# Kernel optimization log

Hardware: AMD Instinct MI355X
Metric: run time of the kernel (lower is better)

The kernel has to match this reference:

```python
import jax, jax.numpy as jnp
import numpy as np
import math


def setup_inputs() -> dict:
    key = jax.random.key(0)
    k1, = jax.random.split(key, 1)
    B, C, N = 64, 128, 4096
    x = jax.random.normal(k1, (B, C, N), dtype=jnp.float32)
    return {
        "x": x,
        "log_peak_width": jnp.asarray(math.log(3.0), dtype=jnp.float32),
        "log_valley_width": jnp.asarray(math.log(3.0), dtype=jnp.float32),
    }


def reference(x, log_peak_width, log_valley_width):
    # x: (B, C, N)
    B, C, N = x.shape
    diff = jnp.diff(x, axis=-1)                      # (B, C, N-1)
    sign_change = jnp.sign(jnp.diff(diff, axis=-1))  # (B, C, N-2)

    # Torch code gathers ALL nonzero positions across (B, C) flattened and sums
    # one gaussian bump per occurrence. Equivalent, jit-friendly form: count
    # occurrences per center position, then weight one gaussian row per center.
    peak_counts = (sign_change < 0).sum(axis=(0, 1)).astype(x.dtype)    # (N-2,)
    valley_counts = (sign_change > 0).sum(axis=(0, 1)).astype(x.dtype)  # (N-2,)

    pos = jnp.arange(N, dtype=x.dtype)               # (N,)
    centers = jnp.arange(1, N - 1, dtype=x.dtype)    # (N-2,) : nonzero index + 1
    dist = pos[None, :] - centers[:, None]           # (N-2, N)

    g_peak = jnp.exp(-(dist / jnp.exp(log_peak_width)) ** 2)
    g_valley = jnp.exp(-(dist / jnp.exp(log_valley_width)) ** 2)
    vec = peak_counts @ g_peak + valley_counts @ g_valley  # (N,)

    attn = jnp.zeros_like(x) + vec                   # broadcast to (B, C, N)
    a_min, a_max = attn.min(), attn.max()
    return (attn - a_min) / (a_max - a_min + 1e-6)
```

## Files before the change

### kernel.cpp

```cpp
#include <hip/hip_runtime.h>

#define N_POS 4096
#define NJ 4094
#define RPB 32

__global__ __launch_bounds__(256) void count_kernel(
    const float* __restrict__ x,
    unsigned int* __restrict__ cnt)
{
    const int tid = threadIdx.x;
    const int j0  = blockIdx.x * 1024 + tid * 4;
    const size_t row0 = (size_t)blockIdx.y * RPB;

    unsigned int pk0 = 0, pk1 = 0, pk2 = 0, pk3 = 0;
    unsigned int vl0 = 0, vl1 = 0, vl2 = 0, vl3 = 0;

    const float* base = x + row0 * N_POS + j0;
    const bool tail = (j0 + 4 >= N_POS);

    #pragma unroll 4
    for (int r = 0; r < RPB; ++r) {
        const float* rowp = base + (size_t)r * N_POS;
        float4 a = *reinterpret_cast<const float4*>(rowp);
        float n0 = 0.f, n1 = 0.f;
        if (!tail) {
            float2 b = *reinterpret_cast<const float2*>(rowp + 4);
            n0 = b.x; n1 = b.y;
        }
        float s;
        s = (a.z - a.y) - (a.y - a.x);
        pk0 += (s < 0.f); vl0 += (s > 0.f);
        s = (a.w - a.z) - (a.z - a.y);
        pk1 += (s < 0.f); vl1 += (s > 0.f);
        s = (n0 - a.w) - (a.w - a.z);
        pk2 += (s < 0.f); vl2 += (s > 0.f);
        s = (n1 - n0) - (n0 - a.w);
        pk3 += (s < 0.f); vl3 += (s > 0.f);
    }

    if (j0 + 0 < NJ) atomicAdd(&cnt[j0 + 0], pk0 | (vl0 << 16));
    if (j0 + 1 < NJ) atomicAdd(&cnt[j0 + 1], pk1 | (vl1 << 16));
    if (j0 + 2 < NJ) atomicAdd(&cnt[j0 + 2], pk2 | (vl2 << 16));
    if (j0 + 3 < NJ) atomicAdd(&cnt[j0 + 3], pk3 | (vl3 << 16));
}

__global__ __launch_bounds__(1024) void vecnorm_kernel(
    const unsigned int* __restrict__ cnt,
    const float* __restrict__ log_pw,
    const float* __restrict__ log_vw,
    float* __restrict__ nvec)
{
    __shared__ float s_pk[NJ];
    __shared__ float s_vl[NJ];
    __shared__ float s_gp[257];
    __shared__ float s_gv[257];
    __shared__ float smin[16], smax[16];

    const int tid = threadIdx.x;
    const float wp = __expf(log_pw[0]);
    const float wv = __expf(log_vw[0]);
    const float ip2 = 1.f / (wp * wp);
    const float iv2 = 1.f / (wv * wv);
    const int Rp = min(128, (int)ceilf(wp * 8.f) + 1);
    const int Rv = min(128, (int)ceilf(wv * 8.f) + 1);

    for (int j = tid; j < NJ; j += 1024) {
        unsigned int c = cnt[j];
        s_pk[j] = (float)(c & 0xFFFFu);
        s_vl[j] = (float)(c >> 16);
    }
    for (int d = tid; d < 257; d += 1024) {
        float dd = (float)(d - 128);
        s_gp[d] = __expf(-dd * dd * ip2);
        s_gv[d] = __expf(-dd * dd * iv2);
    }
    __syncthreads();

    float v[4];
    float lmin = 1e30f, lmax = -1e30f;
    #pragma unroll
    for (int k = 0; k < 4; ++k) {
        const int p = tid + k * 1024;
        float sum = 0.f;
        {
            int clo = max(1, p - Rp), chi = min(NJ, p + Rp);
            for (int c = clo; c <= chi; ++c)
                sum += s_pk[c - 1] * s_gp[p - c + 128];
        }
        {
            int clo = max(1, p - Rv), chi = min(NJ, p + Rv);
            for (int c = clo; c <= chi; ++c)
                sum += s_vl[c - 1] * s_gv[p - c + 128];
        }
        v[k] = sum;
        lmin = fminf(lmin, sum);
        lmax = fmaxf(lmax, sum);
    }

    for (int off = 32; off; off >>= 1) {
        lmin = fminf(lmin, __shfl_down(lmin, off));
        lmax = fmaxf(lmax, __shfl_down(lmax, off));
    }
    const int wave = tid >> 6;
    if ((tid & 63) == 0) { smin[wave] = lmin; smax[wave] = lmax; }
    __syncthreads();
    if (tid == 0) {
        float mn = smin[0], mx = smax[0];
        #pragma unroll
        for (int i = 1; i < 16; ++i) {
            mn = fminf(mn, smin[i]);
            mx = fmaxf(mx, smax[i]);
        }
        smin[0] = mn; smax[0] = mx;
    }
    __syncthreads();
    const float vmin = smin[0];
    const float inv  = 1.f / (smax[0] - vmin + 1e-6f);
    #pragma unroll
    for (int k = 0; k < 4; ++k)
        nvec[tid + k * 1024] = (v[k] - vmin) * inv;
}

__global__ __launch_bounds__(256) void bcast_kernel(
    const float4* __restrict__ nvec4, float4* __restrict__ out4, int total4)
{
    int idx    = blockIdx.x * blockDim.x + threadIdx.x;
    int stride = gridDim.x * blockDim.x;
    for (int i = idx; i < total4; i += stride)
        out4[i] = nvec4[i & 1023];
}

extern "C" void kernel_launch(void* const* d_in, const int* in_sizes, int n_in,
                              void* d_out, int out_size, void* d_ws, size_t ws_size,
                              hipStream_t stream) {
    const float* x   = (const float*)d_in[0];
    const float* lpw = (const float*)d_in[1];
    const float* lvw = (const float*)d_in[2];
    float* out = (float*)d_out;

    unsigned int* cnt = (unsigned int*)d_ws;
    float* nvec = (float*)(cnt + 4096);

    const int rows = in_sizes[0] / N_POS;

    hipMemsetAsync(cnt, 0, 4096 * sizeof(unsigned int), stream);

    dim3 g1(4, rows / RPB);
    count_kernel<<<g1, 256, 0, stream>>>(x, cnt);
    vecnorm_kernel<<<1, 1024, 0, stream>>>(cnt, lpw, lvw, nvec);
    bcast_kernel<<<2048, 256, 0, stream>>>((const float4*)nvec, (float4*)out,
                                           out_size / 4);
}
```

Measured before the change: 266.7 us.

## Split vec computation across blocks, move normalization into broadcast, halve rows per block

The single-block convolution/normalize kernel is replaced by a 16-block kernel. Each block loads only its halo window of counts and publishes its min/max through atomicMax on order-preserving integer encodings. Normalization moves into the broadcast kernel, which reads the global min/max and applies the scale per element. The count kernel now handles 16 rows per block with a fully unrolled loop, which doubles the grid and makes atomics twice as frequent. The goal is to remove the serialized single-block stage at the cost of extra ALU work in the broadcast.

```diff
diff --git a/kernel.cpp b/kernel.cpp
--- a/kernel.cpp
+++ b/kernel.cpp
@@ -2,7 +2,7 @@
 
 #define N_POS 4096
 #define NJ 4094
-#define RPB 32
+#define RPB 16
 
 __global__ __launch_bounds__(256) void count_kernel(
     const float* __restrict__ x,
@@ -18,7 +18,7 @@
     const float* base = x + row0 * N_POS + j0;
     const bool tail = (j0 + 4 >= N_POS);
 
-    #pragma unroll 4
+    #pragma unroll
     for (int r = 0; r < RPB; ++r) {
         const float* rowp = base + (size_t)r * N_POS;
         float4 a = *reinterpret_cast<const float4*>(rowp);
@@ -44,19 +44,22 @@
     if (j0 + 3 < NJ) atomicAdd(&cnt[j0 + 3], pk3 | (vl3 << 16));
 }
 
-__global__ __launch_bounds__(1024) void vecnorm_kernel(
+__global__ __launch_bounds__(256) void vec_kernel(
     const unsigned int* __restrict__ cnt,
     const float* __restrict__ log_pw,
     const float* __restrict__ log_vw,
-    float* __restrict__ nvec)
+    float* __restrict__ vec,
+    unsigned int* __restrict__ mm)
 {
-    __shared__ float s_pk[NJ];
-    __shared__ float s_vl[NJ];
+    __shared__ float s_pk[520];
+    __shared__ float s_vl[520];
     __shared__ float s_gp[257];
     __shared__ float s_gv[257];
-    __shared__ float smin[16], smax[16];
+    __shared__ float smn[4], smx[4];
 
     const int tid = threadIdx.x;
+    const int jb  = blockIdx.x * 256 - 130;
+
     const float wp = __expf(log_pw[0]);
     const float wv = __expf(log_vw[0]);
     const float ip2 = 1.f / (wp * wp);
@@ -64,70 +67,68 @@
     const int Rp = min(128, (int)ceilf(wp * 8.f) + 1);
     const int Rv = min(128, (int)ceilf(wv * 8.f) + 1);
 
-    for (int j = tid; j < NJ; j += 1024) {
-        unsigned int c = cnt[j];
-        s_pk[j] = (float)(c & 0xFFFFu);
-        s_vl[j] = (float)(c >> 16);
+    for (int i = tid; i < 520; i += 256) {
+        int j = jb + i;
+        unsigned int c = (j >= 0 && j < NJ) ? cnt[j] : 0u;
+        s_pk[i] = (float)(c & 0xFFFFu);
+        s_vl[i] = (float)(c >> 16);
     }
-    for (int d = tid; d < 257; d += 1024) {
-        float dd = (float)(d - 128);
-        s_gp[d] = __expf(-dd * dd * ip2);
-        s_gv[d] = __expf(-dd * dd * iv2);
+    for (int i = tid; i < 257; i += 256) {
+        float dd = (float)(i - 128);
+        s_gp[i] = __expf(-dd * dd * ip2);
+        s_gv[i] = __expf(-dd * dd * iv2);
     }
     __syncthreads();
 
-    float v[4];
-    float lmin = 1e30f, lmax = -1e30f;
-    #pragma unroll
-    for (int k = 0; k < 4; ++k) {
-        const int p = tid + k * 1024;
-        float sum = 0.f;
-        {
-            int clo = max(1, p - Rp), chi = min(NJ, p + Rp);
-            for (int c = clo; c <= chi; ++c)
-                sum += s_pk[c - 1] * s_gp[p - c + 128];
-        }
-        {
-            int clo = max(1, p - Rv), chi = min(NJ, p + Rv);
-            for (int c = clo; c <= chi; ++c)
-                sum += s_vl[c - 1] * s_gv[p - c + 128];
-        }
-        v[k] = sum;
-        lmin = fminf(lmin, sum);
-        lmax = fmaxf(lmax, sum);
+    const int p = blockIdx.x * 256 + tid;
+    float sum = 0.f;
+    {
+        int clo = max(1, p - Rp), chi = min(NJ, p + Rp);
+        for (int c = clo; c <= chi; ++c)
+            sum += s_pk[c - 1 - jb] * s_gp[p - c + 128];
     }
+    {
+        int clo = max(1, p - Rv), chi = min(NJ, p + Rv);
+        for (int c = clo; c <= chi; ++c)
+            sum += s_vl[c - 1 - jb] * s_gv[p - c + 128];
+    }
+    vec[p] = sum;
 
+    float mn = sum, mx = sum;
     for (int off = 32; off; off >>= 1) {
-        lmin = fminf(lmin, __shfl_down(lmin, off));
-        lmax = fmaxf(lmax, __shfl_down(lmax, off));
+        mn = fminf(mn, __shfl_down(mn, off));
+        mx = fmaxf(mx, __shfl_down(mx, off));
     }
-    const int wave = tid >> 6;
-    if ((tid & 63) == 0) { smin[wave] = lmin; smax[wave] = lmax; }
+    if ((tid & 63) == 0) { smn[tid >> 6] = mn; smx[tid >> 6] = mx; }
     __syncthreads();
     if (tid == 0) {
-        float mn = smin[0], mx = smax[0];
-        #pragma unroll
-        for (int i = 1; i < 16; ++i) {
-            mn = fminf(mn, smin[i]);
-            mx = fmaxf(mx, smax[i]);
-        }
-        smin[0] = mn; smax[0] = mx;
+        mn = fminf(fminf(smn[0], smn[1]), fminf(smn[2], smn[3]));
+        mx = fmaxf(fmaxf(smx[0], smx[1]), fmaxf(smx[2], smx[3]));
+        atomicMax(&mm[0], 0x7FFFFFFFu - __float_as_uint(mn));
+        atomicMax(&mm[1], __float_as_uint(mx));
     }
-    __syncthreads();
-    const float vmin = smin[0];
-    const float inv  = 1.f / (smax[0] - vmin + 1e-6f);
-    #pragma unroll
-    for (int k = 0; k < 4; ++k)
-        nvec[tid + k * 1024] = (v[k] - vmin) * inv;
 }
 
 __global__ __launch_bounds__(256) void bcast_kernel(
-    const float4* __restrict__ nvec4, float4* __restrict__ out4, int total4)
+    const float4* __restrict__ vec4,
+    const unsigned int* __restrict__ mm,
+    float4* __restrict__ out4, int total4)
 {
+    const float mn  = __uint_as_float(0x7FFFFFFFu - mm[0]);
+    const float mx  = __uint_as_float(mm[1]);
+    const float inv = 1.f / (mx - mn + 1e-6f);
+
     int idx    = blockIdx.x * blockDim.x + threadIdx.x;
     int stride = gridDim.x * blockDim.x;
-    for (int i = idx; i < total4; i += stride)
-        out4[i] = nvec4[i & 1023];
+    for (int i = idx; i < total4; i += stride) {
+        float4 v = vec4[i & 1023];
+        float4 o;
+        o.x = (v.x - mn) * inv;
+        o.y = (v.y - mn) * inv;
+        o.z = (v.z - mn) * inv;
+        o.w = (v.w - mn) * inv;
+        out4[i] = o;
+    }
 }
 
 extern "C" void kernel_launch(void* const* d_in, const int* in_sizes, int n_in,
@@ -139,15 +140,16 @@
     float* out = (float*)d_out;
 
     unsigned int* cnt = (unsigned int*)d_ws;
-    float* nvec = (float*)(cnt + 4096);
+    unsigned int* mm  = cnt + 4096;
+    float* vec = (float*)d_ws + 4352;
 
     const int rows = in_sizes[0] / N_POS;
 
-    hipMemsetAsync(cnt, 0, 4096 * sizeof(unsigned int), stream);
+    hipMemsetAsync(cnt, 0, (4096 + 2) * sizeof(unsigned int), stream);
 
     dim3 g1(4, rows / RPB);
     count_kernel<<<g1, 256, 0, stream>>>(x, cnt);
-    vecnorm_kernel<<<1, 1024, 0, stream>>>(cnt, lpw, lvw, nvec);
-    bcast_kernel<<<2048, 256, 0, stream>>>((const float4*)nvec, (float4*)out,
-                                           out_size / 4);
+    vec_kernel<<<16, 256, 0, stream>>>(cnt, lpw, lvw, vec, mm);
+    bcast_kernel<<<2048, 256, 0, stream>>>((const float4*)vec, mm,
+                                           (float4*)out, out_size / 4);
 }
```

Measured after the change: 259.9 us. 2.5% less time.
